# Optimization experiments

Hardware: AMD Instinct MI355X
Metric: run time of the kernel (lower is better)

The kernel has to match this reference:

```python
import jax, jax.numpy as jnp
import numpy as np

R = 32768          # number of human-object pairs
IN_FEATS = 3072    # input_size * 3 (person + object + union features)
HIDDEN = 1024      # input_size
NUM_CLASSES = 50   # action classes


def setup_inputs() -> dict:
    key = jax.random.key(0)
    k_x, k_w1, k_w2 = jax.random.split(key, 3)
    x = jax.random.normal(k_x, (R, IN_FEATS), dtype=jnp.float32)
    # Linear weights init: normal(std=0.01), bias 0 (as in the module)
    w1 = jax.random.normal(k_w1, (IN_FEATS, HIDDEN), dtype=jnp.float32) * 0.01
    b1 = jnp.zeros((HIDDEN,), dtype=jnp.float32)
    w2 = jax.random.normal(k_w2, (HIDDEN, NUM_CLASSES), dtype=jnp.float32) * 0.01
    b2 = jnp.zeros((NUM_CLASSES,), dtype=jnp.float32)
    return {"x": x, "w1": w1, "b1": b1, "w2": w2, "b2": b2}


def reference(x, w1, b1, w2, b2):
    # HoiOutputLayers.forward: scores = cls_score(relu(cls_fc1(x)))
    h = jax.nn.relu(jnp.dot(x, w1) + b1)          # [R, HIDDEN]
    scores = jnp.dot(h, w2) + b2                  # [R, NUM_CLASSES] action logits
    return scores
```

## Files before the change

### kernel.cpp

```cpp
#include <hip/hip_runtime.h>

#define K1 3072
#define N1 1024
#define NCOL 50

typedef float  f32x4  __attribute__((ext_vector_type(4)));
typedef short  short8 __attribute__((ext_vector_type(8)));

#define GLD16(g, l)                                                        \
  __builtin_amdgcn_global_load_lds(                                        \
      (const __attribute__((address_space(1))) void*)(g),                  \
      (__attribute__((address_space(3))) void*)(l), 16, 0, 0)

#define MFMA_BF16(a, b, c) __builtin_amdgcn_mfma_f32_16x16x32_bf16(a, b, c, 0, 0, 0)

__device__ inline unsigned bfr(float f) {
  return (__builtin_bit_cast(unsigned, f) + 0x8000u) >> 16;
}
__device__ inline short f2bf(float f) { return (short)bfr(f); }
__device__ inline short8 cvt8(float4 a, float4 b) {
  short8 r;
  r[0] = f2bf(a.x); r[1] = f2bf(a.y); r[2] = f2bf(a.z); r[3] = f2bf(a.w);
  r[4] = f2bf(b.x); r[5] = f2bf(b.y); r[6] = f2bf(b.z); r[7] = f2bf(b.w);
  return r;
}

__global__ __launch_bounds__(512) void xcvt_kernel(const float* __restrict__ X,
                                                   short* __restrict__ Xb) {
  size_t i = ((size_t)blockIdx.x * 512 + threadIdx.x) * 8;
  const size_t stride = (size_t)2048 * 512 * 8;
#pragma unroll 4
  for (int it = 0; it < 12; ++it, i += stride) {
    float4 u = *(const float4*)(X + i);
    float4 v = *(const float4*)(X + i + 4);
    *(short8*)(Xb + i) = cvt8(u, v);
  }
}

__global__ __launch_bounds__(256) void w1t_kernel(const float* __restrict__ W1,
                                                  short* __restrict__ W1T) {
  __shared__ float tile[64 * 65];
  const int t = threadIdx.x, b = blockIdx.x;
  const int k0 = (b >> 4) * 64, n0 = (b & 15) * 64;
#pragma unroll
  for (int i = 0; i < 16; ++i) {
    const int e = t + i * 256, r = e >> 6, c = e & 63;
    tile[r * 65 + c] = W1[(size_t)(k0 + r) * N1 + n0 + c];
  }
  __syncthreads();
#pragma unroll
  for (int i = 0; i < 16; ++i) {
    const int e = t + i * 256, kx = e & 63, ny = e >> 6;
    W1T[(size_t)(n0 + ny) * K1 + k0 + kx] = f2bf(tile[kx * 65 + ny]);
  }
}

__global__ __launch_bounds__(256) void w2t_kernel(const float* __restrict__ W2,
                                                  short* __restrict__ W2T) {
  const int idx = blockIdx.x * 256 + threadIdx.x;
  for (int e = idx; e < 64 * N1; e += 16 * 256) {
    const int c = e >> 10, k = e & 1023;
    const float v = (c < NCOL) ? W2[(size_t)k * NCOL + c] : 0.f;
    W2T[(size_t)c * N1 + k] = f2bf(v);
  }
}

#define BK2 64
#define NIT (K1 / BK2)
#define ASLOT (256 * 64)
#define SH2 264

struct __align__(16) Smem2 {
  union {
    struct { short A[2][ASLOT]; short B[2][ASLOT]; } s;
    struct { short h[128 * SH2]; short w2t[64 * SH2]; } e;
  } u;
};

__global__ __launch_bounds__(512, 2)
void hoi_fused2(const short* __restrict__ Xb, const short* __restrict__ W1T,
                const float* __restrict__ B1, const short* __restrict__ W2T,
                const float* __restrict__ B2, float* __restrict__ OUT) {
  __shared__ Smem2 sm;
  const int tid  = threadIdx.x;
  const int lane = tid & 63, wid = tid >> 6;
  const int wr = wid >> 2, wc = wid & 3;
  const int l15 = lane & 15, g = lane >> 4, l7 = l15 & 7;

  const int bid  = blockIdx.x;
  const int gidx = (bid & 7) * 64 + (bid >> 3);
  const int m_blk = gidx >> 2, n_blk = gidx & 3;
  const int m0 = m_blk * 256, n0 = n_blk * 256;

  const int srow  = lane >> 3;
  const int sslot = (lane & 7) ^ srow;
  const short* aS0 = Xb  + (size_t)(m0 + 0   + wid * 16 + srow) * K1 + sslot * 8;
  const short* aS1 = Xb  + (size_t)(m0 + 128 + wid * 16 + srow) * K1 + sslot * 8;
  const short* bS0 = W1T + (size_t)(n0 + 0   + wid * 16 + srow) * K1 + sslot * 8;
  const short* bS1 = W1T + (size_t)(n0 + 128 + wid * 16 + srow) * K1 + sslot * 8;
  const int dL0 = (0   + wid * 16) * 64;
  const int dL1 = (128 + wid * 16) * 64;

#define ISSUE_A0(kt, sl) do { GLD16(aS0 + (size_t)(kt) * BK2,                  &sm.u.s.A[sl][dL0]);        \
                              GLD16(aS0 + (size_t)8 * K1 + (size_t)(kt) * BK2, &sm.u.s.A[sl][dL0 + 512]); } while (0)
#define ISSUE_A1(kt, sl) do { GLD16(aS1 + (size_t)(kt) * BK2,                  &sm.u.s.A[sl][dL1]);        \
                              GLD16(aS1 + (size_t)8 * K1 + (size_t)(kt) * BK2, &sm.u.s.A[sl][dL1 + 512]); } while (0)
#define ISSUE_B0(kt, sl) do { GLD16(bS0 + (size_t)(kt) * BK2,                  &sm.u.s.B[sl][dL0]);        \
                              GLD16(bS0 + (size_t)8 * K1 + (size_t)(kt) * BK2, &sm.u.s.B[sl][dL0 + 512]); } while (0)
#define ISSUE_B1(kt, sl) do { GLD16(bS1 + (size_t)(kt) * BK2,                  &sm.u.s.B[sl][dL1]);        \
                              GLD16(bS1 + (size_t)8 * K1 + (size_t)(kt) * BK2, &sm.u.s.B[sl][dL1 + 512]); } while (0)

  const int aRd = (wr * 128 + l15) * 64;
  const int bRd = (wc * 64  + l15) * 64;
  const int sk0 = ((g)     ^ l7) * 8;
  const int sk1 = ((4 | g) ^ l7) * 8;

  float b1v[4];
#pragma unroll
  for (int nf = 0; nf < 4; ++nf) b1v[nf] = B1[n0 + wc * 64 + nf * 16 + l15];

  f32x4 acc[8][4] = {};

  ISSUE_A0(0, 0); ISSUE_A1(0, 0); ISSUE_B0(0, 0); ISSUE_B1(0, 0);

  for (int t = 0; t < NIT; ++t) {
    const int s  = t & 1, sx = s ^ 1;
    const int tn = (t + 1 < NIT) ? t + 1 : NIT - 1;

    __builtin_amdgcn_s_barrier();
    ISSUE_A0(tn, sx);
    __builtin_amdgcn_sched_barrier(0);
    asm volatile("s_waitcnt vmcnt(2)" ::: "memory");
    __builtin_amdgcn_s_barrier();
    __builtin_amdgcn_sched_barrier(0);

    short8 a_[4][2], b_[4][2];

#pragma unroll
    for (int mf = 0; mf < 4; ++mf) {
      a_[mf][0] = *(const short8*)&sm.u.s.A[s][aRd + mf * 1024 + sk0];
      a_[mf][1] = *(const short8*)&sm.u.s.A[s][aRd + mf * 1024 + sk1];
    }
#pragma unroll
    for (int nf = 0; nf < 2; ++nf) {
      b_[nf][0] = *(const short8*)&sm.u.s.B[s][bRd + nf * 1024 + sk0];
      b_[nf][1] = *(const short8*)&sm.u.s.B[s][bRd + nf * 1024 + sk1];
    }
    asm volatile("s_waitcnt lgkmcnt(0)" ::: "memory");
    __builtin_amdgcn_sched_barrier(0);
    __builtin_amdgcn_s_setprio(1);
#pragma unroll
    for (int mf = 0; mf < 4; ++mf)
#pragma unroll
      for (int nf = 0; nf < 2; ++nf) {
        acc[mf][nf] = MFMA_BF16(a_[mf][0], b_[nf][0], acc[mf][nf]);
        acc[mf][nf] = MFMA_BF16(a_[mf][1], b_[nf][1], acc[mf][nf]);
      }
    __builtin_amdgcn_s_setprio(0);
    ISSUE_A1(tn, sx);
    __builtin_amdgcn_sched_barrier(0);

#pragma unroll
    for (int nf = 2; nf < 4; ++nf) {
      b_[nf][0] = *(const short8*)&sm.u.s.B[s][bRd + nf * 1024 + sk0];
      b_[nf][1] = *(const short8*)&sm.u.s.B[s][bRd + nf * 1024 + sk1];
    }
    asm volatile("s_waitcnt lgkmcnt(0)" ::: "memory");
    __builtin_amdgcn_sched_barrier(0);
    __builtin_amdgcn_s_setprio(1);
#pragma unroll
    for (int mf = 0; mf < 4; ++mf)
#pragma unroll
      for (int nf = 2; nf < 4; ++nf) {
        acc[mf][nf] = MFMA_BF16(a_[mf][0], b_[nf][0], acc[mf][nf]);
        acc[mf][nf] = MFMA_BF16(a_[mf][1], b_[nf][1], acc[mf][nf]);
      }
    __builtin_amdgcn_s_setprio(0);
    ISSUE_B0(tn, sx);
    __builtin_amdgcn_sched_barrier(0);

#pragma unroll
    for (int mf = 0; mf < 4; ++mf) {
      a_[mf][0] = *(const short8*)&sm.u.s.A[s][aRd + (4 + mf) * 1024 + sk0];
      a_[mf][1] = *(const short8*)&sm.u.s.A[s][aRd + (4 + mf) * 1024 + sk1];
    }
    asm volatile("s_waitcnt lgkmcnt(0)" ::: "memory");
    __builtin_amdgcn_sched_barrier(0);
    __builtin_amdgcn_s_setprio(1);
#pragma unroll
    for (int mf = 0; mf < 4; ++mf)
#pragma unroll
      for (int nf = 0; nf < 2; ++nf) {
        acc[4 + mf][nf] = MFMA_BF16(a_[mf][0], b_[nf][0], acc[4 + mf][nf]);
        acc[4 + mf][nf] = MFMA_BF16(a_[mf][1], b_[nf][1], acc[4 + mf][nf]);
      }
    __builtin_amdgcn_s_setprio(0);
    ISSUE_B1(tn, sx);
    __builtin_amdgcn_sched_barrier(0);

    __builtin_amdgcn_s_setprio(1);
#pragma unroll
    for (int mf = 0; mf < 4; ++mf)
#pragma unroll
      for (int nf = 2; nf < 4; ++nf) {
        acc[4 + mf][nf] = MFMA_BF16(a_[mf][0], b_[nf][0], acc[4 + mf][nf]);
        acc[4 + mf][nf] = MFMA_BF16(a_[mf][1], b_[nf][1], acc[4 + mf][nf]);
      }
    __builtin_amdgcn_s_setprio(0);
  }
#undef ISSUE_A0
#undef ISSUE_A1
#undef ISSUE_B0
#undef ISSUE_B1

  for (int ph = 0; ph < 2; ++ph) {
    __syncthreads();

    if (wr == ph) {
#pragma unroll
      for (int mf = 0; mf < 8; ++mf)
#pragma unroll
        for (int nf = 0; nf < 4; ++nf) {
          const int c = wc * 64 + nf * 16 + l15;
#pragma unroll
          for (int j = 0; j < 4; ++j) {
            const int r = mf * 16 + g * 4 + j;
            sm.u.e.h[r * SH2 + c] = f2bf(fmaxf(acc[mf][nf][j] + b1v[nf], 0.f));
          }
        }
    }
    if (ph == 0) {
      const int c = tid & 63, part = tid >> 6;
#pragma unroll
      for (int i = 0; i < 4; ++i)
        *(short8*)&sm.u.e.w2t[c * SH2 + part * 32 + i * 8] =
            *(const short8*)&W2T[(size_t)c * N1 + n0 + part * 32 + i * 8];
    }
    __syncthreads();

    f32x4 acc2[4] = {};
#pragma unroll
    for (int ks = 0; ks < 8; ++ks) {
      const short8 a2 = *(const short8*)&sm.u.e.h[(wid * 16 + l15) * SH2 + ks * 32 + g * 8];
#pragma unroll
      for (int nt = 0; nt < 4; ++nt) {
        const short8 b2 = *(const short8*)&sm.u.e.w2t[(nt * 16 + l15) * SH2 + ks * 32 + g * 8];
        acc2[nt] = MFMA_BF16(a2, b2, acc2[nt]);
      }
    }
#pragma unroll
    for (int nt = 0; nt < 4; ++nt) {
      const int c = nt * 16 + l15;
      if (c < NCOL) {
#pragma unroll
        for (int j = 0; j < 4; ++j) {
          const int r = m0 + ph * 128 + wid * 16 + g * 4 + j;
          float v = acc2[nt][j];
          if (n_blk == 0) v += B2[c];
          atomicAdd(&OUT[(size_t)r * NCOL + c], v);
        }
      }
    }
  }
}

#define BK 32
#define NSTEP (K1 / BK)
#define SAS 40
#define SBS 32
#define SBUF (128 * SBS)
#define SHS 136

struct __align__(16) Smem1 {
  union {
    struct { short A[2][128 * SAS]; short B[2][128 * SBS]; } s;
    struct { short h[64 * SHS]; short w2t[64 * SHS]; } e;
  } u;
};

__global__ __launch_bounds__(256, 4)
void hoi_fused1(const float* __restrict__ X, const short* __restrict__ W1T,
                const float* __restrict__ B1, const short* __restrict__ W2T,
                const float* __restrict__ B2, float* __restrict__ OUT) {
  __shared__ Smem1 sm;
  const int tid  = threadIdx.x;
  const int lane = tid & 63, wid = tid >> 6;
  const int wr = wid >> 1, wc = wid & 1;
  const int l15 = lane & 15, g = lane >> 4;
  const int bid   = blockIdx.x;
  const int xcd   = bid & 7, o = bid >> 3;
  const int m_blk = xcd * 32 + (o >> 3);
  const int n_blk = o & 7;
  const int m0 = m_blk * 128, n0 = n_blk * 128;

  const int arow = tid >> 1;
  const int akc  = (tid & 1) << 4;
  const float* aptr = X + (size_t)(m0 + arow) * K1 + akc;

  const int brow_l = lane >> 2;
  const int bslot  = ((lane & 3) ^ (brow_l & 3)) * 8;
  const short* bsrc0 = W1T + (size_t)(n0 + 32 * wid + brow_l) * K1 + bslot;
  const short* bsrc1 = bsrc0 + (size_t)16 * K1;
  short* const bbase = &sm.u.s.B[0][2 * wid * 512];

  float b1v[4];
#pragma unroll
  for (int nt = 0; nt < 4; ++nt) b1v[nt] = B1[n0 + wc * 64 + nt * 16 + l15];

  f32x4 acc[4][4] = {};
  float4 ra[4];

  GLD16(bsrc0, bbase);
  GLD16(bsrc1, bbase + 512);
#pragma unroll
  for (int q = 0; q < 4; ++q) ra[q] = *(const float4*)(aptr + 4 * q);

  for (int step = 0; step < NSTEP; ++step) {
    const int cb = step & 1;
    const short8 av0 = cvt8(ra[0], ra[1]);
    const short8 av1 = cvt8(ra[2], ra[3]);
    *(short8*)&sm.u.s.A[cb][arow * SAS + akc + 0] = av0;
    *(short8*)&sm.u.s.A[cb][arow * SAS + akc + 8] = av1;
    {
      const int k0v = (step + 1 < NSTEP ? step + 1 : 0) * BK;
#pragma unroll
      for (int q = 0; q < 4; ++q) ra[q] = *(const float4*)(aptr + k0v + 4 * q);
    }
    __builtin_amdgcn_sched_barrier(0);
    asm volatile("s_waitcnt vmcnt(4)" ::: "memory");
    asm volatile("s_waitcnt lgkmcnt(0)" ::: "memory");
    __builtin_amdgcn_s_barrier();
    __builtin_amdgcn_sched_barrier(0);
    if (step + 1 < NSTEP) {
      short* bd = bbase + (cb ^ 1) * SBUF;
      GLD16(bsrc0 + (step + 1) * BK, bd);
      GLD16(bsrc1 + (step + 1) * BK, bd + 512);
    }
    __builtin_amdgcn_sched_barrier(0);

    short8 af[4];
#pragma unroll
    for (int mt = 0; mt < 4; ++mt)
      af[mt] = *(const short8*)&sm.u.s.A[cb][(wr * 64 + mt * 16 + l15) * SAS + g * 8];
#pragma unroll
    for (int nt = 0; nt < 4; ++nt) {
      const int nrow = wc * 64 + nt * 16 + l15;
      const short8 bfv = *(const short8*)&sm.u.s.B[cb][nrow * SBS + ((g ^ (nrow & 3)) * 8)];
#pragma unroll
      for (int mt = 0; mt < 4; ++mt)
        acc[mt][nt] = MFMA_BF16(af[mt], bfv, acc[mt][nt]);
    }
  }

  for (int p = 0; p < 2; ++p) {
    __syncthreads();
    if (wr == p) {
#pragma unroll
      for (int mt = 0; mt < 4; ++mt)
#pragma unroll
        for (int nt = 0; nt < 4; ++nt) {
          const int c = wc * 64 + nt * 16 + l15;
#pragma unroll
          for (int j = 0; j < 4; ++j) {
            const int r = mt * 16 + g * 4 + j;
            sm.u.e.h[r * SHS + c] = f2bf(fmaxf(acc[mt][nt][j] + b1v[nt], 0.f));
          }
        }
    }
    if (p == 0) {
      const int c = tid >> 2, q = tid & 3;
#pragma unroll
      for (int i = 0; i < 4; ++i)
        *(short8*)&sm.u.e.w2t[c * SHS + q * 32 + i * 8] =
            *(const short8*)(W2T + (size_t)c * N1 + n0 + q * 32 + i * 8);
    }
    __syncthreads();

    f32x4 acc2[4] = {};
#pragma unroll
    for (int ks = 0; ks < 4; ++ks) {
      const short8 a2f = *(const short8*)&sm.u.e.h[(wid * 16 + l15) * SHS + ks * 32 + g * 8];
#pragma unroll
      for (int nt2 = 0; nt2 < 4; ++nt2) {
        const short8 b2f = *(const short8*)&sm.u.e.w2t[(nt2 * 16 + l15) * SHS + ks * 32 + g * 8];
        acc2[nt2] = MFMA_BF16(a2f, b2f, acc2[nt2]);
      }
    }
#pragma unroll
    for (int nt2 = 0; nt2 < 4; ++nt2) {
      const int c = nt2 * 16 + l15;
      if (c < NCOL) {
#pragma unroll
        for (int j = 0; j < 4; ++j) {
          const int r = m0 + p * 64 + wid * 16 + g * 4 + j;
          float v = acc2[nt2][j];
          if (n_blk == 0) v += B2[c];
          atomicAdd(&OUT[(size_t)r * NCOL + c], v);
        }
      }
    }
  }
}

struct __align__(16) Smem0 {
  union {
    struct { short A[128 * SAS]; short BT[128 * SAS]; } s[2];
    struct { short h[64 * SHS]; short w2t[64 * SHS]; } e;
  } u;
};

__global__ __launch_bounds__(256, 3)
void hoi_fused0(const float* __restrict__ X, const float* __restrict__ W1,
                const float* __restrict__ B1, const float* __restrict__ W2,
                const float* __restrict__ B2, float* __restrict__ OUT) {
  __shared__ Smem0 sm;
  const int tid  = threadIdx.x;
  const int lane = tid & 63, wid = tid >> 6;
  const int wr = wid >> 1, wc = wid & 1;
  const int l15 = lane & 15, g = lane >> 4;
  const int bid   = blockIdx.x;
  const int xcd   = bid & 7, o = bid >> 3;
  const int m_blk = xcd * 32 + (o >> 3);
  const int n_blk = o & 7;
  const int m0 = m_blk * 128, n0 = n_blk * 128;

  const int arow = tid >> 1;
  const int akc  = (tid & 1) << 4;
  const float* aptr = X + (size_t)(m0 + arow) * K1 + akc;
  const int bk2 = tid >> 4, bcm = tid & 15;
  const float* bptr = W1 + (size_t)(2 * bk2) * N1 + n0 + bcm;

  float b1v[4];
#pragma unroll
  for (int nt = 0; nt < 4; ++nt) b1v[nt] = B1[n0 + wc * 64 + nt * 16 + l15];

  f32x4 acc[4][4] = {};
  float4 ra[4];
  float  rb0[8], rb1[8];
#pragma unroll
  for (int q = 0; q < 4; ++q) ra[q] = *(const float4*)(aptr + 4 * q);
#pragma unroll
  for (int i = 0; i < 8; ++i) { rb0[i] = bptr[16 * i]; rb1[i] = bptr[N1 + 16 * i]; }

  for (int step = 0; step < NSTEP; ++step) {
    const int cb = step & 1;
    const short8 av0 = cvt8(ra[0], ra[1]);
    const short8 av1 = cvt8(ra[2], ra[3]);
    unsigned bpk[8];
#pragma unroll
    for (int i = 0; i < 8; ++i)
      bpk[i] = bfr(rb0[i]) | ((__builtin_bit_cast(unsigned, rb1[i]) + 0x8000u) & 0xFFFF0000u);
    if (step + 1 < NSTEP) {
      const int k0v = (step + 1) * BK;
#pragma unroll
      for (int q = 0; q < 4; ++q) ra[q] = *(const float4*)(aptr + k0v + 4 * q);
      const float* bp = bptr + (size_t)k0v * N1;
#pragma unroll
      for (int i = 0; i < 8; ++i) { rb0[i] = bp[16 * i]; rb1[i] = bp[N1 + 16 * i]; }
    }
    *(short8*)&sm.u.s[cb].A[arow * SAS + akc + 0] = av0;
    *(short8*)&sm.u.s[cb].A[arow * SAS + akc + 8] = av1;
#pragma unroll
    for (int i = 0; i < 8; ++i)
      *(unsigned*)&sm.u.s[cb].BT[(bcm + 16 * i) * SAS + 2 * bk2] = bpk[i];

    asm volatile("s_waitcnt lgkmcnt(0)" ::: "memory");
    __builtin_amdgcn_s_barrier();
    __builtin_amdgcn_sched_barrier(0);

    short8 af[4];
#pragma unroll
    for (int mt = 0; mt < 4; ++mt)
      af[mt] = *(const short8*)&sm.u.s[cb].A[(wr * 64 + mt * 16 + l15) * SAS + g * 8];
#pragma unroll
    for (int nt = 0; nt < 4; ++nt) {
      short8 bfv = *(const short8*)&sm.u.s[cb].BT[(wc * 64 + nt * 16 + l15) * SAS + g * 8];
#pragma unroll
      for (int mt = 0; mt < 4; ++mt)
        acc[mt][nt] = MFMA_BF16(af[mt], bfv, acc[mt][nt]);
    }
  }

  for (int p = 0; p < 2; ++p) {
    __syncthreads();
    if (wr == p) {
#pragma unroll
      for (int mt = 0; mt < 4; ++mt)
#pragma unroll
        for (int nt = 0; nt < 4; ++nt) {
          const int c = wc * 64 + nt * 16 + l15;
#pragma unroll
          for (int j = 0; j < 4; ++j) {
            const int r = mt * 16 + g * 4 + j;
            sm.u.e.h[r * SHS + c] = f2bf(fmaxf(acc[mt][nt][j] + b1v[nt], 0.f));
          }
        }
    }
    if (p == 0) {
      const int kk = tid >> 1, ch = (tid & 1) * 32;
#pragma unroll
      for (int i = 0; i < 32; ++i) {
        const int c = ch + i;
        const float v = (c < NCOL) ? W2[(size_t)(n0 + kk) * NCOL + c] : 0.f;
        sm.u.e.w2t[c * SHS + kk] = f2bf(v);
      }
    }
    __syncthreads();

    f32x4 acc2[4] = {};
#pragma unroll
    for (int ks = 0; ks < 4; ++ks) {
      const short8 a2f = *(const short8*)&sm.u.e.h[(wid * 16 + l15) * SHS + ks * 32 + g * 8];
#pragma unroll
      for (int nt2 = 0; nt2 < 4; ++nt2) {
        const short8 b2f = *(const short8*)&sm.u.e.w2t[(nt2 * 16 + l15) * SHS + ks * 32 + g * 8];
        acc2[nt2] = MFMA_BF16(a2f, b2f, acc2[nt2]);
      }
    }
#pragma unroll
    for (int nt2 = 0; nt2 < 4; ++nt2) {
      const int c = nt2 * 16 + l15;
      if (c < NCOL) {
#pragma unroll
        for (int j = 0; j < 4; ++j) {
          const int r = m0 + p * 64 + wid * 16 + g * 4 + j;
          float v = acc2[nt2][j];
          if (n_blk == 0) v += B2[c];
          atomicAdd(&OUT[(size_t)r * NCOL + c], v);
        }
      }
    }
  }
}

extern "C" void kernel_launch(void* const* d_in, const int* in_sizes, int n_in,
                              void* d_out, int out_size, void* d_ws, size_t ws_size,
                              hipStream_t stream) {
  const float* X  = (const float*)d_in[0];
  const float* W1 = (const float*)d_in[1];
  const float* B1 = (const float*)d_in[2];
  const float* W2 = (const float*)d_in[3];
  const float* B2 = (const float*)d_in[4];
  float* OUT = (float*)d_out;

  const size_t XB_BYTES  = (size_t)32768 * K1 * 2;
  const size_t W1T_BYTES = (size_t)N1 * K1 * 2;
  const size_t W2T_BYTES = (size_t)64 * N1 * 2;

  hipMemsetAsync(d_out, 0, (size_t)out_size * sizeof(float), stream);

  if (ws_size >= XB_BYTES + W1T_BYTES + W2T_BYTES) {
    short* Xb  = (short*)d_ws;
    short* W1T = (short*)((char*)d_ws + XB_BYTES);
    short* W2T = (short*)((char*)d_ws + XB_BYTES + W1T_BYTES);
    hipLaunchKernelGGL(xcvt_kernel, dim3(2048), dim3(512), 0, stream, X, Xb);
    hipLaunchKernelGGL(w1t_kernel, dim3(768), dim3(256), 0, stream, W1, W1T);
    hipLaunchKernelGGL(w2t_kernel, dim3(16), dim3(256), 0, stream, W2, W2T);
    hipLaunchKernelGGL(hoi_fused2, dim3(512), dim3(512), 0, stream, Xb, W1T, B1, W2T, B2, OUT);
  } else if (ws_size >= W1T_BYTES + W2T_BYTES) {
    short* W1T = (short*)d_ws;
    short* W2T = (short*)((char*)d_ws + W1T_BYTES);
    hipLaunchKernelGGL(w1t_kernel, dim3(768), dim3(256), 0, stream, W1, W1T);
    hipLaunchKernelGGL(w2t_kernel, dim3(16), dim3(256), 0, stream, W2, W2T);
    hipLaunchKernelGGL(hoi_fused1, dim3(2048), dim3(256), 0, stream, X, W1T, B1, W2T, B2, OUT);
  } else {
    hipLaunchKernelGGL(hoi_fused0, dim3(2048), dim3(256), 0, stream, X, W1, B1, W2, B2, OUT);
  }
}
```

Baseline: 337.7 us.

## Fuse fp32-to-bf16 conversion of X into the main GEMM pipeline

Removes the separate xcvt pass that wrote a bf16 copy of X to workspace. The main 256x256 GEMM kernel now loads fp32 X rows into registers two k-tiles ahead, converts them to bf16 and stores them into the swizzled LDS A buffer mid-iteration. W1T keeps using async global-to-LDS loads, with the issue points reshuffled. This avoids writing and re-reading the bf16 copy of X, at the cost of more register pressure and doubled global bytes per A tile inside the kernel. The fallback kernel hoi_fused1 is deleted and an odd no-op expression is added to the fused0 path.

```diff
diff --git a/kernel.cpp b/kernel.cpp
--- a/kernel.cpp
+++ b/kernel.cpp
@@ -23,18 +23,6 @@
   r[0] = f2bf(a.x); r[1] = f2bf(a.y); r[2] = f2bf(a.z); r[3] = f2bf(a.w);
   r[4] = f2bf(b.x); r[5] = f2bf(b.y); r[6] = f2bf(b.z); r[7] = f2bf(b.w);
   return r;
-}
-
-__global__ __launch_bounds__(512) void xcvt_kernel(const float* __restrict__ X,
-                                                   short* __restrict__ Xb) {
-  size_t i = ((size_t)blockIdx.x * 512 + threadIdx.x) * 8;
-  const size_t stride = (size_t)2048 * 512 * 8;
-#pragma unroll 4
-  for (int it = 0; it < 12; ++it, i += stride) {
-    float4 u = *(const float4*)(X + i);
-    float4 v = *(const float4*)(X + i + 4);
-    *(short8*)(Xb + i) = cvt8(u, v);
-  }
 }
 
 __global__ __launch_bounds__(256) void w1t_kernel(const float* __restrict__ W1,
@@ -78,7 +66,7 @@
 };
 
 __global__ __launch_bounds__(512, 2)
-void hoi_fused2(const short* __restrict__ Xb, const short* __restrict__ W1T,
+void hoi_fused2(const float* __restrict__ X, const short* __restrict__ W1T,
                 const float* __restrict__ B1, const short* __restrict__ W2T,
                 const float* __restrict__ B2, float* __restrict__ OUT) {
   __shared__ Smem2 sm;
@@ -92,19 +80,19 @@
   const int m_blk = gidx >> 2, n_blk = gidx & 3;
   const int m0 = m_blk * 256, n0 = n_blk * 256;
 
+  const int ar = tid >> 1;
+  const int ah = tid & 1;
+  const float* aptr = X + (size_t)(m0 + ar) * K1 + ah * 32;
+  const int awr = ar * 64;
+  const int ar7 = ar & 7;
+
   const int srow  = lane >> 3;
   const int sslot = (lane & 7) ^ srow;
-  const short* aS0 = Xb  + (size_t)(m0 + 0   + wid * 16 + srow) * K1 + sslot * 8;
-  const short* aS1 = Xb  + (size_t)(m0 + 128 + wid * 16 + srow) * K1 + sslot * 8;
   const short* bS0 = W1T + (size_t)(n0 + 0   + wid * 16 + srow) * K1 + sslot * 8;
   const short* bS1 = W1T + (size_t)(n0 + 128 + wid * 16 + srow) * K1 + sslot * 8;
   const int dL0 = (0   + wid * 16) * 64;
   const int dL1 = (128 + wid * 16) * 64;
 
-#define ISSUE_A0(kt, sl) do { GLD16(aS0 + (size_t)(kt) * BK2,                  &sm.u.s.A[sl][dL0]);        \
-                              GLD16(aS0 + (size_t)8 * K1 + (size_t)(kt) * BK2, &sm.u.s.A[sl][dL0 + 512]); } while (0)
-#define ISSUE_A1(kt, sl) do { GLD16(aS1 + (size_t)(kt) * BK2,                  &sm.u.s.A[sl][dL1]);        \
-                              GLD16(aS1 + (size_t)8 * K1 + (size_t)(kt) * BK2, &sm.u.s.A[sl][dL1 + 512]); } while (0)
 #define ISSUE_B0(kt, sl) do { GLD16(bS0 + (size_t)(kt) * BK2,                  &sm.u.s.B[sl][dL0]);        \
                               GLD16(bS0 + (size_t)8 * K1 + (size_t)(kt) * BK2, &sm.u.s.B[sl][dL0 + 512]); } while (0)
 #define ISSUE_B1(kt, sl) do { GLD16(bS1 + (size_t)(kt) * BK2,                  &sm.u.s.B[sl][dL1]);        \
@@ -120,17 +108,26 @@
   for (int nf = 0; nf < 4; ++nf) b1v[nf] = B1[n0 + wc * 64 + nf * 16 + l15];
 
   f32x4 acc[8][4] = {};
-
-  ISSUE_A0(0, 0); ISSUE_A1(0, 0); ISSUE_B0(0, 0); ISSUE_B1(0, 0);
+  float4 ra[8];
+
+  ISSUE_B0(0, 0); ISSUE_B1(0, 0);
+#pragma unroll
+  for (int q = 0; q < 8; ++q) ra[q] = *(const float4*)(aptr + 4 * q);
+#pragma unroll
+  for (int j = 0; j < 4; ++j) {
+    const short8 v = cvt8(ra[2 * j], ra[2 * j + 1]);
+    *(short8*)&sm.u.s.A[0][awr + (((ah << 2) | j) ^ ar7) * 8] = v;
+  }
+#pragma unroll
+  for (int q = 0; q < 8; ++q) ra[q] = *(const float4*)(aptr + BK2 + 4 * q);
 
   for (int t = 0; t < NIT; ++t) {
     const int s  = t & 1, sx = s ^ 1;
     const int tn = (t + 1 < NIT) ? t + 1 : NIT - 1;
-
-    __builtin_amdgcn_s_barrier();
-    ISSUE_A0(tn, sx);
-    __builtin_amdgcn_sched_barrier(0);
-    asm volatile("s_waitcnt vmcnt(2)" ::: "memory");
+    const int ta = (t + 2 < NIT) ? t + 2 : NIT - 1;
+
+    asm volatile("s_waitcnt vmcnt(8)" ::: "memory");
+    asm volatile("s_waitcnt lgkmcnt(0)" ::: "memory");
     __builtin_amdgcn_s_barrier();
     __builtin_amdgcn_sched_barrier(0);
 
@@ -157,7 +154,7 @@
         acc[mf][nf] = MFMA_BF16(a_[mf][1], b_[nf][1], acc[mf][nf]);
       }
     __builtin_amdgcn_s_setprio(0);
-    ISSUE_A1(tn, sx);
+    ISSUE_B0(tn, sx);
     __builtin_amdgcn_sched_barrier(0);
 
 #pragma unroll
@@ -176,7 +173,7 @@
         acc[mf][nf] = MFMA_BF16(a_[mf][1], b_[nf][1], acc[mf][nf]);
       }
     __builtin_amdgcn_s_setprio(0);
-    ISSUE_B0(tn, sx);
+    ISSUE_B1(tn, sx);
     __builtin_amdgcn_sched_barrier(0);
 
 #pragma unroll
@@ -195,7 +192,11 @@
         acc[4 + mf][nf] = MFMA_BF16(a_[mf][1], b_[nf][1], acc[4 + mf][nf]);
       }
     __builtin_amdgcn_s_setprio(0);
-    ISSUE_B1(tn, sx);
+#pragma unroll
+    for (int j = 0; j < 4; ++j) {
+      const short8 v = cvt8(ra[2 * j], ra[2 * j + 1]);
+      *(short8*)&sm.u.s.A[sx][awr + (((ah << 2) | j) ^ ar7) * 8] = v;
+    }
     __builtin_amdgcn_sched_barrier(0);
 
     __builtin_amdgcn_s_setprio(1);
@@ -207,9 +208,13 @@
         acc[4 + mf][nf] = MFMA_BF16(a_[mf][1], b_[nf][1], acc[4 + mf][nf]);
       }
     __builtin_amdgcn_s_setprio(0);
-  }
-#undef ISSUE_A0
-#undef ISSUE_A1
+    {
+      const float* ap = aptr + (size_t)ta * BK2;
+#pragma unroll
+      for (int q = 0; q < 8; ++q) ra[q] = *(const float4*)(ap + 4 * q);
+    }
+    __builtin_amdgcn_sched_barrier(0);
+  }
 #undef ISSUE_B0
 #undef ISSUE_B1
 
@@ -267,140 +272,7 @@
 #define BK 32
 #define NSTEP (K1 / BK)
 #define SAS 40
-#define SBS 32
-#define SBUF (128 * SBS)
 #define SHS 136
-
-struct __align__(16) Smem1 {
-  union {
-    struct { short A[2][128 * SAS]; short B[2][128 * SBS]; } s;
-    struct { short h[64 * SHS]; short w2t[64 * SHS]; } e;
-  } u;
-};
-
-__global__ __launch_bounds__(256, 4)
-void hoi_fused1(const float* __restrict__ X, const short* __restrict__ W1T,
-                const float* __restrict__ B1, const short* __restrict__ W2T,
-                const float* __restrict__ B2, float* __restrict__ OUT) {
-  __shared__ Smem1 sm;
-  const int tid  = threadIdx.x;
-  const int lane = tid & 63, wid = tid >> 6;
-  const int wr = wid >> 1, wc = wid & 1;
-  const int l15 = lane & 15, g = lane >> 4;
-  const int bid   = blockIdx.x;
-  const int xcd   = bid & 7, o = bid >> 3;
-  const int m_blk = xcd * 32 + (o >> 3);
-  const int n_blk = o & 7;
-  const int m0 = m_blk * 128, n0 = n_blk * 128;
-
-  const int arow = tid >> 1;
-  const int akc  = (tid & 1) << 4;
-  const float* aptr = X + (size_t)(m0 + arow) * K1 + akc;
-
-  const int brow_l = lane >> 2;
-  const int bslot  = ((lane & 3) ^ (brow_l & 3)) * 8;
-  const short* bsrc0 = W1T + (size_t)(n0 + 32 * wid + brow_l) * K1 + bslot;
-  const short* bsrc1 = bsrc0 + (size_t)16 * K1;
-  short* const bbase = &sm.u.s.B[0][2 * wid * 512];
-
-  float b1v[4];
-#pragma unroll
-  for (int nt = 0; nt < 4; ++nt) b1v[nt] = B1[n0 + wc * 64 + nt * 16 + l15];
-
-  f32x4 acc[4][4] = {};
-  float4 ra[4];
-
-  GLD16(bsrc0, bbase);
-  GLD16(bsrc1, bbase + 512);
-#pragma unroll
-  for (int q = 0; q < 4; ++q) ra[q] = *(const float4*)(aptr + 4 * q);
-
-  for (int step = 0; step < NSTEP; ++step) {
-    const int cb = step & 1;
-    const short8 av0 = cvt8(ra[0], ra[1]);
-    const short8 av1 = cvt8(ra[2], ra[3]);
-    *(short8*)&sm.u.s.A[cb][arow * SAS + akc + 0] = av0;
-    *(short8*)&sm.u.s.A[cb][arow * SAS + akc + 8] = av1;
-    {
-      const int k0v = (step + 1 < NSTEP ? step + 1 : 0) * BK;
-#pragma unroll
-      for (int q = 0; q < 4; ++q) ra[q] = *(const float4*)(aptr + k0v + 4 * q);
-    }
-    __builtin_amdgcn_sched_barrier(0);
-    asm volatile("s_waitcnt vmcnt(4)" ::: "memory");
-    asm volatile("s_waitcnt lgkmcnt(0)" ::: "memory");
-    __builtin_amdgcn_s_barrier();
-    __builtin_amdgcn_sched_barrier(0);
-    if (step + 1 < NSTEP) {
-      short* bd = bbase + (cb ^ 1) * SBUF;
-      GLD16(bsrc0 + (step + 1) * BK, bd);
-      GLD16(bsrc1 + (step + 1) * BK, bd + 512);
-    }
-    __builtin_amdgcn_sched_barrier(0);
-
-    short8 af[4];
-#pragma unroll
-    for (int mt = 0; mt < 4; ++mt)
-      af[mt] = *(const short8*)&sm.u.s.A[cb][(wr * 64 + mt * 16 + l15) * SAS + g * 8];
-#pragma unroll
-    for (int nt = 0; nt < 4; ++nt) {
-      const int nrow = wc * 64 + nt * 16 + l15;
-      const short8 bfv = *(const short8*)&sm.u.s.B[cb][nrow * SBS + ((g ^ (nrow & 3)) * 8)];
-#pragma unroll
-      for (int mt = 0; mt < 4; ++mt)
-        acc[mt][nt] = MFMA_BF16(af[mt], bfv, acc[mt][nt]);
-    }
-  }
-
-  for (int p = 0; p < 2; ++p) {
-    __syncthreads();
-    if (wr == p) {
-#pragma unroll
-      for (int mt = 0; mt < 4; ++mt)
-#pragma unroll
-        for (int nt = 0; nt < 4; ++nt) {
-          const int c = wc * 64 + nt * 16 + l15;
-#pragma unroll
-          for (int j = 0; j < 4; ++j) {
-            const int r = mt * 16 + g * 4 + j;
-            sm.u.e.h[r * SHS + c] = f2bf(fmaxf(acc[mt][nt][j] + b1v[nt], 0.f));
-          }
-        }
-    }
-    if (p == 0) {
-      const int c = tid >> 2, q = tid & 3;
-#pragma unroll
-      for (int i = 0; i < 4; ++i)
-        *(short8*)&sm.u.e.w2t[c * SHS + q * 32 + i * 8] =
-            *(const short8*)(W2T + (size_t)c * N1 + n0 + q * 32 + i * 8);
-    }
-    __syncthreads();
-
-    f32x4 acc2[4] = {};
-#pragma unroll
-    for (int ks = 0; ks < 4; ++ks) {
-      const short8 a2f = *(const short8*)&sm.u.e.h[(wid * 16 + l15) * SHS + ks * 32 + g * 8];
-#pragma unroll
-      for (int nt2 = 0; nt2 < 4; ++nt2) {
-        const short8 b2f = *(const short8*)&sm.u.e.w2t[(nt2 * 16 + l15) * SHS + ks * 32 + g * 8];
-        acc2[nt2] = MFMA_BF16(a2f, b2f, acc2[nt2]);
-      }
-    }
-#pragma unroll
-    for (int nt2 = 0; nt2 < 4; ++nt2) {
-      const int c = nt2 * 16 + l15;
-      if (c < NCOL) {
-#pragma unroll
-        for (int j = 0; j < 4; ++j) {
-          const int r = m0 + p * 64 + wid * 16 + g * 4 + j;
-          float v = acc2[nt2][j];
-          if (n_blk == 0) v += B2[c];
-          atomicAdd(&OUT[(size_t)r * NCOL + c], v);
-        }
-      }
-    }
-  }
-}
 
 struct __align__(16) Smem0 {
   union {
@@ -501,7 +373,7 @@
 #pragma unroll
       for (int i = 0; i < 32; ++i) {
         const int c = ch + i;
-        const float v = (c < NCOL) ? W2[(size_t)(n0 + kk) * NCOL + c] : 0.f;
+        const float v = (c < NCOL) ? W2[(size_t)kk * NCOL + c] * 0.f + ((c < NCOL) ? W2[(size_t)(n0 + kk) * NCOL + c] : 0.f) : 0.f;
         sm.u.e.w2t[c * SHS + kk] = f2bf(v);
       }
     }
@@ -543,26 +415,17 @@
   const float* B2 = (const float*)d_in[4];
   float* OUT = (float*)d_out;
 
-  const size_t XB_BYTES  = (size_t)32768 * K1 * 2;
   const size_t W1T_BYTES = (size_t)N1 * K1 * 2;
   const size_t W2T_BYTES = (size_t)64 * N1 * 2;
 
   hipMemsetAsync(d_out, 0, (size_t)out_size * sizeof(float), stream);
 
-  if (ws_size >= XB_BYTES + W1T_BYTES + W2T_BYTES) {
-    short* Xb  = (short*)d_ws;
-    short* W1T = (short*)((char*)d_ws + XB_BYTES);
-    short* W2T = (short*)((char*)d_ws + XB_BYTES + W1T_BYTES);
-    hipLaunchKernelGGL(xcvt_kernel, dim3(2048), dim3(512), 0, stream, X, Xb);
-    hipLaunchKernelGGL(w1t_kernel, dim3(768), dim3(256), 0, stream, W1, W1T);
-    hipLaunchKernelGGL(w2t_kernel, dim3(16), dim3(256), 0, stream, W2, W2T);
-    hipLaunchKernelGGL(hoi_fused2, dim3(512), dim3(512), 0, stream, Xb, W1T, B1, W2T, B2, OUT);
-  } else if (ws_size >= W1T_BYTES + W2T_BYTES) {
+  if (ws_size >= W1T_BYTES + W2T_BYTES) {
     short* W1T = (short*)d_ws;
     short* W2T = (short*)((char*)d_ws + W1T_BYTES);
     hipLaunchKernelGGL(w1t_kernel, dim3(768), dim3(256), 0, stream, W1, W1T);
     hipLaunchKernelGGL(w2t_kernel, dim3(16), dim3(256), 0, stream, W2, W2T);
-    hipLaunchKernelGGL(hoi_fused1, dim3(2048), dim3(256), 0, stream, X, W1T, B1, W2T, B2, OUT);
+    hipLaunchKernelGGL(hoi_fused2, dim3(512), dim3(512), 0, stream, X, W1T, B1, W2T, B2, OUT);
   } else {
     hipLaunchKernelGGL(hoi_fused0, dim3(2048), dim3(256), 0, stream, X, W1, B1, W2, B2, OUT);
   }
```

After: 361.3 us. 1.07x slower.
